# Kernel tuning notes

Measured on AMD Instinct MI355X. Metric: run time of the kernel, lower is better.

## Reference

```python
import jax, jax.numpy as jnp
import numpy as np

NUM_HEADS = 8

def rotate_half(x):
    # interleaved rotate: pairs (x0,x1)->(-x1,x0)
    x1 = x[..., ::2]
    x2 = x[..., 1::2]
    return jnp.stack((-x2, x1), axis=-1).reshape(x.shape)

def rope_cos_sin(seq_len, head_dim, dtype, base=10000.0):
    idx = jnp.arange(0, head_dim, 2, dtype=dtype)
    inv_freq = 1.0 / base ** (idx / head_dim)
    t = jnp.arange(seq_len, dtype=dtype)
    freqs = t[:, None] * inv_freq[None, :]            # (L, hd/2)
    emb = jnp.concatenate([freqs, freqs], axis=-1)    # (L, hd) -- NOTE: cat, not interleave (faithful to source)
    return jnp.cos(emb)[None, None], jnp.sin(emb)[None, None]  # (1,1,L,hd)

def setup_inputs() -> dict:
    key = jax.random.key(0)
    ks = jax.random.split(key, 5)
    B, L, C = 2, 4096, 512
    s_in = 1.0 / np.sqrt(C)
    return {
        "x": jax.random.normal(ks[0], (B, L, C), dtype=jnp.float32),
        "qkv_w": jax.random.normal(ks[1], (3 * C, C), dtype=jnp.float32) * s_in,
        "qkv_b": jnp.zeros((3 * C,), dtype=jnp.float32),
        "proj_w": jax.random.normal(ks[2], (C, C), dtype=jnp.float32) * s_in,
        "proj_b": jnp.zeros((C,), dtype=jnp.float32),
    }

def reference(x, qkv_w, qkv_b, proj_w, proj_b):
    B, L, C = x.shape
    H = NUM_HEADS
    hd = C // H
    scale = hd ** -0.5
    qkv = x @ qkv_w.T + qkv_b                          # (B,L,3C)
    qkv = qkv.reshape(B, L, 3, H, hd).transpose(2, 0, 3, 1, 4)  # (3,B,H,L,hd)
    q, k, v = qkv[0], qkv[1], qkv[2]
    cos, sin = rope_cos_sin(L, hd, x.dtype)
    q = q * cos + rotate_half(q) * sin
    k = k * cos + rotate_half(k) * sin
    attn = jnp.einsum('bhqd,bhkd->bhqk', q, k) * scale  # (B,H,L,L)
    attn = jax.nn.softmax(attn, axis=-1)
    out = jnp.einsum('bhqk,bhkd->bhqd', attn, v)        # (B,H,L,hd)
    out = out.transpose(0, 2, 1, 3).reshape(B, L, C)
    return out @ proj_w.T + proj_b
```

## Files before the change

kernel.cpp:

```cpp
#include <hip/hip_runtime.h>
#include <hip/hip_bf16.h>


typedef __attribute__((ext_vector_type(8)))  short short8;
typedef __attribute__((ext_vector_type(4)))  short short4v;
typedef __attribute__((ext_vector_type(4)))  float floatx4;
typedef __attribute__((ext_vector_type(16))) float floatx16;

#define MFMA(a, b, c)   __builtin_amdgcn_mfma_f32_16x16x32_bf16((a), (b), (c), 0, 0, 0)
#define MFMA32(a, b, c) __builtin_amdgcn_mfma_f32_32x32x16_bf16((a), (b), (c), 0, 0, 0)

__device__ __forceinline__ float fast_exp2(float x) {
#if __has_builtin(__builtin_amdgcn_exp2f)
    return __builtin_amdgcn_exp2f(x);
#else
    float r; asm("v_exp_f32 %0, %1" : "=v"(r) : "v"(x)); return r;
#endif
}

__device__ __forceinline__ unsigned short f2bf(float f) {
    unsigned int u = __builtin_bit_cast(unsigned int, f);
    return (unsigned short)((u + 0x7fffu + ((u >> 16) & 1u)) >> 16);
}
__device__ __forceinline__ unsigned int pack2(float lo, float hi) {
    __hip_bfloat162 h = __float22bfloat162_rn(make_float2(lo, hi));
    unsigned int r;
    __builtin_memcpy(&r, &h, 4);
    return r;
}

__global__ __launch_bounds__(256) void conv_pack(
    const float* __restrict__ src, ushort* __restrict__ dst, int n8)
{
    int i = blockIdx.x * blockDim.x + threadIdx.x;
    if (i >= n8) return;
    const int row = i >> 6, col0 = (i & 63) * 8;
    const float4* s = (const float4*)(src + (size_t)row * 512 + col0);
    float4 a = s[0], b = s[1];
    uint4 r = { pack2(a.x, a.y), pack2(a.z, a.w), pack2(b.x, b.y), pack2(b.z, b.w) };
    const int l = (row & 15) + 16 * ((col0 >> 3) & 3);
    const size_t off = (size_t)(row >> 4) * 8192 + (size_t)(col0 >> 5) * 512 + l * 8;
    *(uint4*)(dst + off) = r;
}

__global__ __launch_bounds__(256) void build_rope(float2* __restrict__ lut) {
    int i = blockIdx.x * 256 + threadIdx.x;
    int pos = i >> 5, j = i & 31;
    float invf = exp2f(-0.41524101186f * (float)j);
    float s, c;
    sincosf((float)pos * invf, &s, &c);
    lut[i] = make_float2(c, s);
}

__global__ __launch_bounds__(256) void qkv_rope(
    const ushort* __restrict__ xb,
    const ushort* __restrict__ wb,
    const float* __restrict__ bias,
    const float2* __restrict__ lut,
    ushort* __restrict__ q, ushort* __restrict__ k, ushort* __restrict__ vt,
    int G, int h0)
{
    __shared__ __align__(16) ushort vtile[64][136];
    const int w_id = threadIdx.x >> 6;
    const int lane = threadIdx.x & 63;
    const int lr = lane & 15, quad = lane >> 4;
    const int m0 = blockIdx.x * 128 + w_id * 32;
    const int sec = blockIdx.y / G, hl = blockIdx.y % G;
    const int wc0 = sec * 512 + (h0 + hl) * 64;

    floatx4 acc[2][4] = {};
    const ushort* xa = xb + (size_t)(m0 >> 4) * 8192 + lane * 8;
    const ushort* wbase = wb + (size_t)(wc0 >> 4) * 8192 + lane * 8;
    for (int kk = 0; kk < 16; ++kk) {
        short8 a0 = *(const short8*)(xa + kk * 512);
        short8 a1 = *(const short8*)(xa + 8192 + kk * 512);
#pragma unroll
        for (int nt = 0; nt < 4; ++nt) {
            short8 b = *(const short8*)(wbase + (size_t)nt * 8192 + kk * 512);
            acc[0][nt] = MFMA(a0, b, acc[0][nt]);
            acc[1][nt] = MFMA(a1, b, acc[1][nt]);
        }
    }

    if (sec < 2) {
#pragma unroll
        for (int mt = 0; mt < 2; ++mt)
#pragma unroll
            for (int nt = 0; nt < 4; ++nt) {
                const int d = nt * 16 + lr;
                const float bv = bias[wc0 + d];
#pragma unroll
                for (int r = 0; r < 4; ++r) {
                    const int row = m0 + mt * 16 + quad * 4 + r;
                    const int b_ = row >> 12;
                    const int pos = row & 4095;
                    float val = acc[mt][nt][r] + bv;
                    const size_t bhl = (size_t)(b_ * G + hl);
                    float partner = __shfl_xor(val, 1);
                    float2 cs = lut[(pos << 5) | (d & 31)];
                    float rh = (d & 1) ? partner : -partner;
                    float rv = val * cs.x + rh * cs.y;
                    if (sec == 0) {
                        rv *= 0.18033688011112042f;
                        q[(bhl * 4096 + pos) * 64 + d] = f2bf(rv);
                    } else {
                        const int idx = (pos >> 5) * 2048 + (d >> 4) * 512
                                      + ((pos & 31) + 32 * ((d >> 3) & 1)) * 8
                                      + (d & 7);
                        k[bhl * 262144 + idx] = f2bf(rv);
                    }
                }
            }
    } else {
#pragma unroll
        for (int mt = 0; mt < 2; ++mt)
#pragma unroll
            for (int nt = 0; nt < 4; ++nt) {
                const int d = nt * 16 + lr;
                const float bv = bias[wc0 + d];
                short4v v4;
#pragma unroll
                for (int r = 0; r < 4; ++r)
                    v4[r] = (short)f2bf(acc[mt][nt][r] + bv);
                *(short4v*)&vtile[d][w_id * 32 + mt * 16 + quad * 4] = v4;
            }
        __syncthreads();
        const int m0b = blockIdx.x * 128;
        const int bb = m0b >> 12;
        const int c0g = (m0b & 4095) >> 5;
        const size_t bhl = (size_t)(bb * G + hl);
        const int gid = threadIdx.x >> 6;
        const int l = threadIdx.x & 63;
        const int h = l >> 5;
        ushort* vb = vt + bhl * 262144 + l * 8;
#pragma unroll
        for (int i = 0; i < 4; ++i) {
            const int combo = i * 4 + gid;
            const int c4 = combo >> 2, dt = (combo >> 1) & 1, s = combo & 1;
            const int d = dt * 32 + (l & 31);
            const int colbase = c4 * 32 + s * 16 + 4 * h;
            short4v a = *(const short4v*)&vtile[d][colbase];
            short4v b = *(const short4v*)&vtile[d][colbase + 8];
            short8 vv = __builtin_shufflevector(a, b, 0, 1, 2, 3, 4, 5, 6, 7);
            *(short8*)(vb + (size_t)(c0g + c4) * 2048 + dt * 1024 + s * 512) = vv;
        }
    }
}

__global__ __launch_bounds__(256, 2) void flash_attn(
    const ushort* __restrict__ q, const ushort* __restrict__ k,
    const ushort* __restrict__ vt, ushort* __restrict__ o,
    int G, int h0)
{
    __shared__ __align__(16) ushort kv[2][4096];
    const int w_id = threadIdx.x >> 6;
    const int lane = threadIdx.x & 63;
    const int ln31 = lane & 31, h = lane >> 5;
    const int nbh = 2 * G;
    const int bhl = blockIdx.x % nbh;
    const int qt = blockIdx.x / nbh;
    const int b_ = bhl / G, hl = bhl % G;
    const int q0 = qt * 128 + w_id * 32;

    const ushort* qp = q + (size_t)bhl * 262144;
    const ushort* kp = k + (size_t)bhl * 262144;
    const ushort* vp = vt + (size_t)bhl * 262144;
    const int hcol = (h0 + hl) * 64;
    ushort* opp = o + (size_t)(((b_ << 12) + q0) >> 4) * 8192 + (hcol >> 5) * 512;

    const ushort* stsrc = ((w_id < 2) ? kp : vp) + (w_id & 1) * 1024 + lane * 8;
    const int stdst = w_id * 1024 + lane * 8;

    short8 qf[4];
    {
        const ushort* qb = qp + (size_t)(q0 + ln31) * 64 + h * 8;
        qf[0] = *(const short8*)(qb);
        qf[1] = *(const short8*)(qb + 16);
        qf[2] = *(const short8*)(qb + 32);
        qf[3] = *(const short8*)(qb + 48);
    }

    floatx16 oacc[2] = {};
    float lsum = 0.f;

    auto process = [&](int cur) {
        const ushort* kb = &kv[cur][lane * 8];
        short8 ka0 = *(const short8*)(kb);
        short8 ka1 = *(const short8*)(kb + 512);
        short8 ka2 = *(const short8*)(kb + 1024);
        short8 ka3 = *(const short8*)(kb + 1536);
        const ushort* vb = kb + 2048;
        short8 va0 = *(const short8*)(vb);
        short8 va1 = *(const short8*)(vb + 512);
        short8 va2 = *(const short8*)(vb + 1024);
        short8 va3 = *(const short8*)(vb + 1536);
        floatx16 s = {};
        s = MFMA32(ka0, qf[0], s);
        s = MFMA32(ka1, qf[1], s);
        s = MFMA32(ka2, qf[2], s);
        s = MFMA32(ka3, qf[3], s);
        float p[16];
#pragma unroll
        for (int r = 0; r < 16; ++r) p[r] = fast_exp2(s[r]);
        float t0 = (p[0] + p[1]) + (p[2] + p[3]);
        float t1 = (p[4] + p[5]) + (p[6] + p[7]);
        float t2 = (p[8] + p[9]) + (p[10] + p[11]);
        float t3 = (p[12] + p[13]) + (p[14] + p[15]);
        lsum += (t0 + t1) + (t2 + t3);
        uint4 u0 = { pack2(p[0], p[1]), pack2(p[2], p[3]),
                     pack2(p[4], p[5]), pack2(p[6], p[7]) };
        uint4 u1 = { pack2(p[8], p[9]), pack2(p[10], p[11]),
                     pack2(p[12], p[13]), pack2(p[14], p[15]) };
        short8 pb0 = __builtin_bit_cast(short8, u0);
        short8 pb1 = __builtin_bit_cast(short8, u1);
        oacc[0] = MFMA32(va0, pb0, oacc[0]);
        oacc[0] = MFMA32(va1, pb1, oacc[0]);
        oacc[1] = MFMA32(va2, pb0, oacc[1]);
        oacc[1] = MFMA32(va3, pb1, oacc[1]);
    };

    {
        short8 t0 = *(const short8*)(stsrc);
        short8 t1 = *(const short8*)(stsrc + 512);
        *(short8*)(&kv[0][stdst]) = t0;
        *(short8*)(&kv[0][stdst + 512]) = t1;
    }
    __syncthreads();

    int cur = 0;
    for (int c = 0; c < 127; ++c) {
        const ushort* src = stsrc + (c + 1) * 2048;
        short8 t0 = *(const short8*)(src);
        short8 t1 = *(const short8*)(src + 512);
        process(cur);
        *(short8*)(&kv[cur ^ 1][stdst]) = t0;
        *(short8*)(&kv[cur ^ 1][stdst + 512]) = t1;
        __syncthreads();
        cur ^= 1;
    }
    process(cur);

    lsum += __shfl_xor(lsum, 32);

    const float inv = 1.0f / lsum;
#pragma unroll
    for (int dt = 0; dt < 2; ++dt)
#pragma unroll
        for (int g = 0; g < 4; ++g) {
            float v0 = oacc[dt][4 * g + 0] * inv;
            float v1 = oacc[dt][4 * g + 1] * inv;
            float v2 = oacc[dt][4 * g + 2] * inv;
            float v3 = oacc[dt][4 * g + 3] * inv;
            uint2 u = { pack2(v0, v1), pack2(v2, v3) };
            *(uint2*)(opp + (size_t)(ln31 >> 4) * 8192 + dt * 512
                      + ((ln31 & 15) + 16 * g) * 8 + 4 * h) = u;
        }
}

__global__ __launch_bounds__(256) void proj_gemm(
    const ushort* __restrict__ o,
    const ushort* __restrict__ wb,
    const float* __restrict__ bias,
    float* __restrict__ out)
{
    const int w_id = threadIdx.x >> 6;
    const int lane = threadIdx.x & 63;
    const int lr = lane & 15, quad = lane >> 4;
    const int m0 = blockIdx.x * 128 + w_id * 32;
    const int n0 = blockIdx.y * 64;

    floatx4 acc[2][4] = {};
    const ushort* oa = o + (size_t)(m0 >> 4) * 8192 + lane * 8;
    const ushort* wbase = wb + (size_t)(n0 >> 4) * 8192 + lane * 8;
    for (int kk = 0; kk < 16; ++kk) {
        short8 a0 = *(const short8*)(oa + kk * 512);
        short8 a1 = *(const short8*)(oa + 8192 + kk * 512);
#pragma unroll
        for (int nt = 0; nt < 4; ++nt) {
            short8 b = *(const short8*)(wbase + (size_t)nt * 8192 + kk * 512);
            acc[0][nt] = MFMA(a0, b, acc[0][nt]);
            acc[1][nt] = MFMA(a1, b, acc[1][nt]);
        }
    }
#pragma unroll
    for (int mt = 0; mt < 2; ++mt)
#pragma unroll
        for (int nt = 0; nt < 4; ++nt) {
            const int n = n0 + nt * 16 + lr;
            const float bv = bias[n];
#pragma unroll
            for (int r = 0; r < 4; ++r)
                out[(size_t)(m0 + mt * 16 + quad * 4 + r) * 512 + n] = acc[mt][nt][r] + bv;
        }
}

extern "C" void kernel_launch(void* const* d_in, const int* in_sizes, int n_in,
                              void* d_out, int out_size, void* d_ws, size_t ws_size,
                              hipStream_t stream)
{
    const float* x      = (const float*)d_in[0];
    const float* qkv_w  = (const float*)d_in[1];
    const float* qkv_b  = (const float*)d_in[2];
    const float* proj_w = (const float*)d_in[3];
    const float* proj_b = (const float*)d_in[4];
    float* out = (float*)d_out;

    const size_t MB = (size_t)1 << 20;
    ushort* base = (ushort*)d_ws;
    int G;
    ushort *xb, *o, *wb, *pwb, *q, *k, *vt;
    if (ws_size >= 34 * MB) {
        G = 8;
        xb = base; o = base;
        wb  = base + 4194304;
        pwb = wb + 786432;
        q   = pwb + 262144;
        k   = q + (size_t)G * 524288;
        vt  = k + (size_t)G * 524288;
    } else {
        G = (ws_size >= 30 * MB) ? 4 : (ws_size >= 24 * MB) ? 2 : 1;
        xb  = base;
        o   = base + 4194304;
        wb  = o + 4194304;
        pwb = wb + 786432;
        q   = pwb + 262144;
        k   = q + (size_t)G * 524288;
        vt  = k + (size_t)G * 524288;
    }

    float2* lut = (float2*)d_out;
    build_rope<<<512, 256, 0, stream>>>(lut);

    conv_pack<<<2048, 256, 0, stream>>>(x, xb, 524288);
    conv_pack<<<384, 256, 0, stream>>>(qkv_w, wb, 98304);
    conv_pack<<<128, 256, 0, stream>>>(proj_w, pwb, 32768);

    for (int h0 = 0; h0 < 8; h0 += G) {
        qkv_rope<<<dim3(64, 3 * G), 256, 0, stream>>>(xb, wb, qkv_b, lut, q, k, vt, G, h0);
        flash_attn<<<32 * 2 * G, 256, 0, stream>>>(q, k, vt, o, G, h0);
    }
    proj_gemm<<<dim3(64, 8), 256, 0, stream>>>(o, pwb, proj_b, out);
}
```

Measured before the change: 210.8 us.

## Software-pipeline attention loop: overlap previous PV MFMAs with current QK and exp

Restructures the KV loop so the P·V MFMAs for tile c-1 are issued alongside the QK^T MFMAs and exp2 work for tile c. The V fragments and packed P from the previous iteration are carried in registers across the barrier. The intent is to hide the latency of the exp and pack chain behind independent MFMA work. In exchange it raises register pressure and adds explicit prologue and epilogue code.

Result: faster. 202.6 us (-3.9%).

```diff
diff --git a/kernel.cpp b/kernel.cpp
--- a/kernel.cpp
+++ b/kernel.cpp
@@ -182,18 +182,20 @@
 
     floatx16 oacc[2] = {};
     float lsum = 0.f;
-
-    auto process = [&](int cur) {
+    short8 vp0, vp1, vp2, vp3;
+    short8 pb0, pb1;
+
+    auto qk_exp = [&](int cur, short8& vn0, short8& vn1, short8& vn2, short8& vn3) {
         const ushort* kb = &kv[cur][lane * 8];
         short8 ka0 = *(const short8*)(kb);
         short8 ka1 = *(const short8*)(kb + 512);
         short8 ka2 = *(const short8*)(kb + 1024);
         short8 ka3 = *(const short8*)(kb + 1536);
         const ushort* vb = kb + 2048;
-        short8 va0 = *(const short8*)(vb);
-        short8 va1 = *(const short8*)(vb + 512);
-        short8 va2 = *(const short8*)(vb + 1024);
-        short8 va3 = *(const short8*)(vb + 1536);
+        vn0 = *(const short8*)(vb);
+        vn1 = *(const short8*)(vb + 512);
+        vn2 = *(const short8*)(vb + 1024);
+        vn3 = *(const short8*)(vb + 1536);
         floatx16 s = {};
         s = MFMA32(ka0, qf[0], s);
         s = MFMA32(ka1, qf[1], s);
@@ -211,12 +213,14 @@
                      pack2(p[4], p[5]), pack2(p[6], p[7]) };
         uint4 u1 = { pack2(p[8], p[9]), pack2(p[10], p[11]),
                      pack2(p[12], p[13]), pack2(p[14], p[15]) };
-        short8 pb0 = __builtin_bit_cast(short8, u0);
-        short8 pb1 = __builtin_bit_cast(short8, u1);
-        oacc[0] = MFMA32(va0, pb0, oacc[0]);
-        oacc[0] = MFMA32(va1, pb1, oacc[0]);
-        oacc[1] = MFMA32(va2, pb0, oacc[1]);
-        oacc[1] = MFMA32(va3, pb1, oacc[1]);
+        pb0 = __builtin_bit_cast(short8, u0);
+        pb1 = __builtin_bit_cast(short8, u1);
+    };
+    auto pv = [&](short8 a0, short8 a1, short8 a2, short8 a3) {
+        oacc[0] = MFMA32(a0, pb0, oacc[0]);
+        oacc[0] = MFMA32(a1, pb1, oacc[0]);
+        oacc[1] = MFMA32(a2, pb0, oacc[1]);
+        oacc[1] = MFMA32(a3, pb1, oacc[1]);
     };
 
     {
@@ -227,18 +231,92 @@
     }
     __syncthreads();
 
-    int cur = 0;
-    for (int c = 0; c < 127; ++c) {
+    {
+        const ushort* src = stsrc + 2048;
+        short8 t0 = *(const short8*)(src);
+        short8 t1 = *(const short8*)(src + 512);
+        qk_exp(0, vp0, vp1, vp2, vp3);
+        *(short8*)(&kv[1][stdst]) = t0;
+        *(short8*)(&kv[1][stdst + 512]) = t1;
+        __syncthreads();
+    }
+
+    for (int c = 1; c < 127; ++c) {
+        const int cur = c & 1;
         const ushort* src = stsrc + (c + 1) * 2048;
         short8 t0 = *(const short8*)(src);
         short8 t1 = *(const short8*)(src + 512);
-        process(cur);
+        short8 vn0, vn1, vn2, vn3;
+        const ushort* kb = &kv[cur][lane * 8];
+        short8 ka0 = *(const short8*)(kb);
+        short8 ka1 = *(const short8*)(kb + 512);
+        short8 ka2 = *(const short8*)(kb + 1024);
+        short8 ka3 = *(const short8*)(kb + 1536);
+        const ushort* vb = kb + 2048;
+        vn0 = *(const short8*)(vb);
+        vn1 = *(const short8*)(vb + 512);
+        vn2 = *(const short8*)(vb + 1024);
+        vn3 = *(const short8*)(vb + 1536);
+        pv(vp0, vp1, vp2, vp3);
+        floatx16 s = {};
+        s = MFMA32(ka0, qf[0], s);
+        s = MFMA32(ka1, qf[1], s);
+        s = MFMA32(ka2, qf[2], s);
+        s = MFMA32(ka3, qf[3], s);
+        float p[16];
+#pragma unroll
+        for (int r = 0; r < 16; ++r) p[r] = fast_exp2(s[r]);
+        float u0s = (p[0] + p[1]) + (p[2] + p[3]);
+        float u1s = (p[4] + p[5]) + (p[6] + p[7]);
+        float u2s = (p[8] + p[9]) + (p[10] + p[11]);
+        float u3s = (p[12] + p[13]) + (p[14] + p[15]);
+        lsum += (u0s + u1s) + (u2s + u3s);
+        uint4 w0 = { pack2(p[0], p[1]), pack2(p[2], p[3]),
+                     pack2(p[4], p[5]), pack2(p[6], p[7]) };
+        uint4 w1 = { pack2(p[8], p[9]), pack2(p[10], p[11]),
+                     pack2(p[12], p[13]), pack2(p[14], p[15]) };
+        pb0 = __builtin_bit_cast(short8, w0);
+        pb1 = __builtin_bit_cast(short8, w1);
+        vp0 = vn0; vp1 = vn1; vp2 = vn2; vp3 = vn3;
         *(short8*)(&kv[cur ^ 1][stdst]) = t0;
         *(short8*)(&kv[cur ^ 1][stdst + 512]) = t1;
         __syncthreads();
-        cur ^= 1;
-    }
-    process(cur);
+    }
+
+    {
+        short8 vn0, vn1, vn2, vn3;
+        const ushort* kb = &kv[1][lane * 8];
+        short8 ka0 = *(const short8*)(kb);
+        short8 ka1 = *(const short8*)(kb + 512);
+        short8 ka2 = *(const short8*)(kb + 1024);
+        short8 ka3 = *(const short8*)(kb + 1536);
+        const ushort* vb = kb + 2048;
+        vn0 = *(const short8*)(vb);
+        vn1 = *(const short8*)(vb + 512);
+        vn2 = *(const short8*)(vb + 1024);
+        vn3 = *(const short8*)(vb + 1536);
+        pv(vp0, vp1, vp2, vp3);
+        floatx16 s = {};
+        s = MFMA32(ka0, qf[0], s);
+        s = MFMA32(ka1, qf[1], s);
+        s = MFMA32(ka2, qf[2], s);
+        s = MFMA32(ka3, qf[3], s);
+        float p[16];
+#pragma unroll
+        for (int r = 0; r < 16; ++r) p[r] = fast_exp2(s[r]);
+        float u0s = (p[0] + p[1]) + (p[2] + p[3]);
+        float u1s = (p[4] + p[5]) + (p[6] + p[7]);
+        float u2s = (p[8] + p[9]) + (p[10] + p[11]);
+        float u3s = (p[12] + p[13]) + (p[14] + p[15]);
+        lsum += (u0s + u1s) + (u2s + u3s);
+        uint4 w0 = { pack2(p[0], p[1]), pack2(p[2], p[3]),
+                     pack2(p[4], p[5]), pack2(p[6], p[7]) };
+        uint4 w1 = { pack2(p[8], p[9]), pack2(p[10], p[11]),
+                     pack2(p[12], p[13]), pack2(p[14], p[15]) };
+        pb0 = __builtin_bit_cast(short8, w0);
+        pb1 = __builtin_bit_cast(short8, w1);
+        pv(vn0, vn1, vn2, vn3);
+    }
 
     lsum += __shfl_xor(lsum, 32);
 
```

## Software-pipeline flash attention over paired KV chunks and tile Q/K stores

Applied to the files above, without the earlier changes.

The attention loop now stages two 32-key chunks per barrier in a four-buffer LDS ring. It interleaves QK MFMAs, softmax and deferred PV MFMAs across chunks so matrix work overlaps exp/pack work, and it halves the number of barriers. The QKV projection now writes Q and K through an LDS tile as coalesced 16-byte stores in a fragment-ready layout, and Q fragments are loaded with contiguous reads. The cost is more LDS per block and more live registers, which may reduce occupancy.

Measured after the change: 206.2 us. 2.2% less time.

```diff
diff --git a/kernel.cpp b/kernel.cpp
--- a/kernel.cpp
+++ b/kernel.cpp
@@ -60,7 +60,7 @@
     ushort* __restrict__ q, ushort* __restrict__ k, ushort* __restrict__ vt,
     int G, int h0)
 {
-    __shared__ __align__(16) ushort vtile[64][136];
+    __shared__ __align__(16) ushort tl[9216];
     const int w_id = threadIdx.x >> 6;
     const int lane = threadIdx.x & 63;
     const int lr = lane & 15, quad = lane >> 4;
@@ -82,6 +82,11 @@
         }
     }
 
+    const int m0b = blockIdx.x * 128;
+    const int bb = m0b >> 12;
+    const int pos0 = m0b & 4095;
+    const size_t bhl = (size_t)(bb * G + hl);
+
     if (sec < 2) {
 #pragma unroll
         for (int mt = 0; mt < 2; ++mt)
@@ -91,26 +96,27 @@
                 const float bv = bias[wc0 + d];
 #pragma unroll
                 for (int r = 0; r < 4; ++r) {
-                    const int row = m0 + mt * 16 + quad * 4 + r;
-                    const int b_ = row >> 12;
-                    const int pos = row & 4095;
+                    const int pl = w_id * 32 + mt * 16 + quad * 4 + r;
+                    const int pos = pos0 + pl;
                     float val = acc[mt][nt][r] + bv;
-                    const size_t bhl = (size_t)(b_ * G + hl);
                     float partner = __shfl_xor(val, 1);
                     float2 cs = lut[(pos << 5) | (d & 31)];
                     float rh = (d & 1) ? partner : -partner;
                     float rv = val * cs.x + rh * cs.y;
-                    if (sec == 0) {
-                        rv *= 0.18033688011112042f;
-                        q[(bhl * 4096 + pos) * 64 + d] = f2bf(rv);
-                    } else {
-                        const int idx = (pos >> 5) * 2048 + (d >> 4) * 512
-                                      + ((pos & 31) + 32 * ((d >> 3) & 1)) * 8
-                                      + (d & 7);
-                        k[bhl * 262144 + idx] = f2bf(rv);
-                    }
+                    if (sec == 0) rv *= 0.18033688011112042f;
+                    tl[pl * 72 + d] = f2bf(rv);
                 }
             }
+        __syncthreads();
+        ushort* dst = ((sec == 0) ? q : k) + bhl * 262144 + (pos0 >> 5) * 2048;
+#pragma unroll
+        for (int i = 0; i < 4; ++i) {
+            const int combo = i * 4 + w_id;
+            const int c4 = combo >> 2, ks = combo & 3;
+            short8 vv = *(const short8*)&tl[(c4 * 32 + (lane & 31)) * 72
+                                            + ks * 16 + (lane >> 5) * 8];
+            *(short8*)(dst + c4 * 2048 + ks * 512 + lane * 8) = vv;
+        }
     } else {
 #pragma unroll
         for (int mt = 0; mt < 2; ++mt)
@@ -122,15 +128,12 @@
 #pragma unroll
                 for (int r = 0; r < 4; ++r)
                     v4[r] = (short)f2bf(acc[mt][nt][r] + bv);
-                *(short4v*)&vtile[d][w_id * 32 + mt * 16 + quad * 4] = v4;
+                *(short4v*)&tl[d * 136 + w_id * 32 + mt * 16 + quad * 4] = v4;
             }
         __syncthreads();
-        const int m0b = blockIdx.x * 128;
-        const int bb = m0b >> 12;
-        const int c0g = (m0b & 4095) >> 5;
-        const size_t bhl = (size_t)(bb * G + hl);
-        const int gid = threadIdx.x >> 6;
-        const int l = threadIdx.x & 63;
+        const int c0g = pos0 >> 5;
+        const int gid = w_id;
+        const int l = lane;
         const int h = l >> 5;
         ushort* vb = vt + bhl * 262144 + l * 8;
 #pragma unroll
@@ -139,8 +142,8 @@
             const int c4 = combo >> 2, dt = (combo >> 1) & 1, s = combo & 1;
             const int d = dt * 32 + (l & 31);
             const int colbase = c4 * 32 + s * 16 + 4 * h;
-            short4v a = *(const short4v*)&vtile[d][colbase];
-            short4v b = *(const short4v*)&vtile[d][colbase + 8];
+            short4v a = *(const short4v*)&tl[d * 136 + colbase];
+            short4v b = *(const short4v*)&tl[d * 136 + colbase + 8];
             short8 vv = __builtin_shufflevector(a, b, 0, 1, 2, 3, 4, 5, 6, 7);
             *(short8*)(vb + (size_t)(c0g + c4) * 2048 + dt * 1024 + s * 512) = vv;
         }
@@ -152,7 +155,7 @@
     const ushort* __restrict__ vt, ushort* __restrict__ o,
     int G, int h0)
 {
-    __shared__ __align__(16) ushort kv[2][4096];
+    __shared__ __align__(16) ushort kv[4][4096];
     const int w_id = threadIdx.x >> 6;
     const int lane = threadIdx.x & 63;
     const int ln31 = lane & 31, h = lane >> 5;
@@ -164,41 +167,42 @@
 
     const ushort* qp = q + (size_t)bhl * 262144;
     const ushort* kp = k + (size_t)bhl * 262144;
-    const ushort* vp = vt + (size_t)bhl * 262144;
+    const ushort* vp_ = vt + (size_t)bhl * 262144;
     const int hcol = (h0 + hl) * 64;
     ushort* opp = o + (size_t)(((b_ << 12) + q0) >> 4) * 8192 + (hcol >> 5) * 512;
 
-    const ushort* stsrc = ((w_id < 2) ? kp : vp) + (w_id & 1) * 1024 + lane * 8;
+    const ushort* stsrc = ((w_id < 2) ? kp : vp_) + (w_id & 1) * 1024 + lane * 8;
     const int stdst = w_id * 1024 + lane * 8;
 
     short8 qf[4];
     {
-        const ushort* qb = qp + (size_t)(q0 + ln31) * 64 + h * 8;
+        const ushort* qb = qp + (q0 >> 5) * 2048 + lane * 8;
         qf[0] = *(const short8*)(qb);
-        qf[1] = *(const short8*)(qb + 16);
-        qf[2] = *(const short8*)(qb + 32);
-        qf[3] = *(const short8*)(qb + 48);
+        qf[1] = *(const short8*)(qb + 512);
+        qf[2] = *(const short8*)(qb + 1024);
+        qf[3] = *(const short8*)(qb + 1536);
     }
 
     floatx16 oacc[2] = {};
     float lsum = 0.f;
-
-    auto process = [&](int cur) {
-        const ushort* kb = &kv[cur][lane * 8];
-        short8 ka0 = *(const short8*)(kb);
-        short8 ka1 = *(const short8*)(kb + 512);
-        short8 ka2 = *(const short8*)(kb + 1024);
-        short8 ka3 = *(const short8*)(kb + 1536);
-        const ushort* vb = kb + 2048;
-        short8 va0 = *(const short8*)(vb);
-        short8 va1 = *(const short8*)(vb + 512);
-        short8 va2 = *(const short8*)(vb + 1024);
-        short8 va3 = *(const short8*)(vb + 1536);
+    short8 pb0, pb1;
+    short8 vp0, vp1, vp2, vp3;
+
+    auto ldfr = [&](const ushort* b, short8& f0, short8& f1, short8& f2, short8& f3) {
+        f0 = *(const short8*)(b);
+        f1 = *(const short8*)(b + 512);
+        f2 = *(const short8*)(b + 1024);
+        f3 = *(const short8*)(b + 1536);
+    };
+    auto qk32 = [&](short8 a0, short8 a1, short8 a2, short8 a3) {
         floatx16 s = {};
-        s = MFMA32(ka0, qf[0], s);
-        s = MFMA32(ka1, qf[1], s);
-        s = MFMA32(ka2, qf[2], s);
-        s = MFMA32(ka3, qf[3], s);
+        s = MFMA32(a0, qf[0], s);
+        s = MFMA32(a1, qf[1], s);
+        s = MFMA32(a2, qf[2], s);
+        s = MFMA32(a3, qf[3], s);
+        return s;
+    };
+    auto smax = [&](const floatx16& s) {
         float p[16];
 #pragma unroll
         for (int r = 0; r < 16; ++r) p[r] = fast_exp2(s[r]);
@@ -211,34 +215,92 @@
                      pack2(p[4], p[5]), pack2(p[6], p[7]) };
         uint4 u1 = { pack2(p[8], p[9]), pack2(p[10], p[11]),
                      pack2(p[12], p[13]), pack2(p[14], p[15]) };
-        short8 pb0 = __builtin_bit_cast(short8, u0);
-        short8 pb1 = __builtin_bit_cast(short8, u1);
-        oacc[0] = MFMA32(va0, pb0, oacc[0]);
-        oacc[0] = MFMA32(va1, pb1, oacc[0]);
-        oacc[1] = MFMA32(va2, pb0, oacc[1]);
-        oacc[1] = MFMA32(va3, pb1, oacc[1]);
+        pb0 = __builtin_bit_cast(short8, u0);
+        pb1 = __builtin_bit_cast(short8, u1);
+    };
+    auto pv = [&](short8 a0, short8 a1, short8 a2, short8 a3) {
+        oacc[0] = MFMA32(a0, pb0, oacc[0]);
+        oacc[0] = MFMA32(a1, pb1, oacc[0]);
+        oacc[1] = MFMA32(a2, pb0, oacc[1]);
+        oacc[1] = MFMA32(a3, pb1, oacc[1]);
     };
 
     {
         short8 t0 = *(const short8*)(stsrc);
         short8 t1 = *(const short8*)(stsrc + 512);
+        short8 t2 = *(const short8*)(stsrc + 2048);
+        short8 t3 = *(const short8*)(stsrc + 2048 + 512);
         *(short8*)(&kv[0][stdst]) = t0;
         *(short8*)(&kv[0][stdst + 512]) = t1;
+        *(short8*)(&kv[1][stdst]) = t2;
+        *(short8*)(&kv[1][stdst + 512]) = t3;
     }
     __syncthreads();
 
-    int cur = 0;
-    for (int c = 0; c < 127; ++c) {
-        const ushort* src = stsrc + (c + 1) * 2048;
+    {
+        const ushort* src = stsrc + 2 * 2048;
         short8 t0 = *(const short8*)(src);
         short8 t1 = *(const short8*)(src + 512);
-        process(cur);
-        *(short8*)(&kv[cur ^ 1][stdst]) = t0;
-        *(short8*)(&kv[cur ^ 1][stdst + 512]) = t1;
+        short8 t2 = *(const short8*)(src + 2048);
+        short8 t3 = *(const short8*)(src + 2048 + 512);
+        short8 ka0, ka1, ka2, ka3, kb0, kb1, kb2, kb3, va0, va1, va2, va3;
+        ldfr(&kv[0][lane * 8], ka0, ka1, ka2, ka3);
+        ldfr(&kv[0][lane * 8 + 2048], va0, va1, va2, va3);
+        ldfr(&kv[1][lane * 8], kb0, kb1, kb2, kb3);
+        floatx16 s0 = qk32(ka0, ka1, ka2, ka3);
+        floatx16 s1 = qk32(kb0, kb1, kb2, kb3);
+        smax(s0);
+        pv(va0, va1, va2, va3);
+        ldfr(&kv[1][lane * 8 + 2048], vp0, vp1, vp2, vp3);
+        smax(s1);
+        *(short8*)(&kv[2][stdst]) = t0;
+        *(short8*)(&kv[2][stdst + 512]) = t1;
+        *(short8*)(&kv[3][stdst]) = t2;
+        *(short8*)(&kv[3][stdst + 512]) = t3;
         __syncthreads();
-        cur ^= 1;
-    }
-    process(cur);
+    }
+
+    for (int w = 1; w < 63; ++w) {
+        const int pr = (w & 1) * 2;
+        const ushort* src = stsrc + (2 * w + 2) * 2048;
+        short8 t0 = *(const short8*)(src);
+        short8 t1 = *(const short8*)(src + 512);
+        short8 t2 = *(const short8*)(src + 2048);
+        short8 t3 = *(const short8*)(src + 2048 + 512);
+        short8 ka0, ka1, ka2, ka3, kb0, kb1, kb2, kb3, va0, va1, va2, va3;
+        ldfr(&kv[pr][lane * 8], ka0, ka1, ka2, ka3);
+        ldfr(&kv[pr][lane * 8 + 2048], va0, va1, va2, va3);
+        ldfr(&kv[pr + 1][lane * 8], kb0, kb1, kb2, kb3);
+        pv(vp0, vp1, vp2, vp3);
+        floatx16 s0 = qk32(ka0, ka1, ka2, ka3);
+        floatx16 s1 = qk32(kb0, kb1, kb2, kb3);
+        smax(s0);
+        pv(va0, va1, va2, va3);
+        ldfr(&kv[pr + 1][lane * 8 + 2048], vp0, vp1, vp2, vp3);
+        smax(s1);
+        const int op = pr ^ 2;
+        *(short8*)(&kv[op][stdst]) = t0;
+        *(short8*)(&kv[op][stdst + 512]) = t1;
+        *(short8*)(&kv[op + 1][stdst]) = t2;
+        *(short8*)(&kv[op + 1][stdst + 512]) = t3;
+        __syncthreads();
+    }
+
+    {
+        short8 ka0, ka1, ka2, ka3, kb0, kb1, kb2, kb3;
+        short8 va0, va1, va2, va3, vb0, vb1, vb2, vb3;
+        ldfr(&kv[2][lane * 8], ka0, ka1, ka2, ka3);
+        ldfr(&kv[2][lane * 8 + 2048], va0, va1, va2, va3);
+        ldfr(&kv[3][lane * 8], kb0, kb1, kb2, kb3);
+        ldfr(&kv[3][lane * 8 + 2048], vb0, vb1, vb2, vb3);
+        pv(vp0, vp1, vp2, vp3);
+        floatx16 s0 = qk32(ka0, ka1, ka2, ka3);
+        floatx16 s1 = qk32(kb0, kb1, kb2, kb3);
+        smax(s0);
+        pv(va0, va1, va2, va3);
+        smax(s1);
+        pv(vb0, vb1, vb2, vb3);
+    }
 
     lsum += __shfl_xor(lsum, 32);
 
```
